# Kernel optimization log

Measured on AMD Instinct MI355X. Metric: run time of the kernel, lower is better.

The kernel has to match this reference:

```python
import jax, jax.numpy as jnp
import numpy as np

B, T, D, H, E, S, K = 2, 2048, 768, 1536, 8, 1, 2
STD = 0.02


def setup_inputs() -> dict:
    key = jax.random.key(0)
    ks = jax.random.split(key, 8)
    x = jax.random.normal(ks[0], (B, T, D), jnp.float32)
    router_w = jax.random.normal(ks[1], (E, D), jnp.float32) * STD
    sw1 = jax.random.normal(ks[2], (S, D, H), jnp.float32) * STD
    sw2 = jax.random.normal(ks[3], (S, D, H), jnp.float32) * STD
    sproj = jax.random.normal(ks[4], (S, H, D), jnp.float32) * STD
    ew1 = jax.random.normal(ks[5], (E, D, H), jnp.float32) * STD
    ew2 = jax.random.normal(ks[6], (E, D, H), jnp.float32) * STD
    eproj = jax.random.normal(ks[7], (E, H, D), jnp.float32) * STD
    return {"x": x, "router_w": router_w, "sw1": sw1, "sw2": sw2,
            "sproj": sproj, "ew1": ew1, "ew2": ew2, "eproj": eproj,
            "top_k": K}


def reference(x, router_w, sw1, sw2, sproj, ew1, ew2, eproj, top_k):
    n_experts = router_w.shape[0]
    # Shared experts (SwiGLU), summed over the shared-expert axis s.
    a = jnp.einsum('btd,sdh->bsth', x, sw1)
    b = jnp.einsum('btd,sdh->bsth', x, sw2)
    shared_out = jnp.einsum('bsth,shd->btd', jax.nn.silu(a) * b, sproj)  # [B,T,D]

    # Router: note the original applies softmax and calls the result `logits`,
    # returning it as the second output.
    probs = jax.nn.softmax(jnp.einsum('btd,ed->bte', x, router_w), axis=-1)  # [B,T,E]
    top_vals, top_idx = jax.lax.top_k(probs, top_k)
    weights = top_vals / jnp.sum(top_vals, axis=-1, keepdims=True)  # renormalized [B,T,K]

    # Dense combine weights: combine[b,t,e] = sum_k weights[b,t,k] * 1[top_idx[b,t,k]==e]
    combine = jnp.sum(jax.nn.one_hot(top_idx, n_experts, dtype=x.dtype)
                      * weights[..., None], axis=-2)  # [B,T,E]

    # Routed experts: compute every expert densely, then mask/weight by combine.
    ea = jnp.einsum('btd,edh->bteh', x, ew1)
    eb = jnp.einsum('btd,edh->bteh', x, ew2)
    routed = jnp.einsum('bteh,ehd,bte->btd', jax.nn.silu(ea) * eb, eproj, combine)

    return shared_out + routed, probs
```

## Files before the change

### kernel.cpp

```cpp
#include <hip/hip_runtime.h>

typedef unsigned short u16;
typedef __bf16 bf16x8 __attribute__((ext_vector_type(8)));
typedef float f32x4 __attribute__((ext_vector_type(4)));

__device__ __forceinline__ u16 f2bf(float f) {
  union { float f; unsigned u; } v; v.f = f;
  return (u16)((v.u + 0x7fffu + ((v.u >> 16) & 1u)) >> 16);
}

#define GLDS16(g, l)                                                          \
  __builtin_amdgcn_global_load_lds(                                           \
      (const __attribute__((address_space(1))) void*)(g),                     \
      (__attribute__((address_space(3))) void*)(l), 16, 0, 0)

#define SBAR()  __builtin_amdgcn_s_barrier()
#define SCHED() __builtin_amdgcn_sched_barrier(0)
#define VMCNT(n) asm volatile("s_waitcnt vmcnt(" #n ")" ::: "memory")

#define NTOK 4096
#define DIM  768
#define HID  1536
#define NEXP 8
#define CAPR 10240
#define SHB  10240
#define NSLOT 14336
#define MAXT1 56
#define MAXT2 112

__global__ __launch_bounds__(256) void k_tr_all(const float* __restrict__ ew1,
                                                const float* __restrict__ sw1,
                                                const float* __restrict__ ew2,
                                                const float* __restrict__ sw2,
                                                const float* __restrict__ eproj,
                                                const float* __restrict__ sproj,
                                                u16* __restrict__ dstBase) {
  __shared__ u16 tile[64][65];
  constexpr size_t SL = (size_t)HID * DIM;
  const int z = blockIdx.z;
  const float* src;
  int R, C, bxx = blockIdx.x, byy = blockIdx.y;
  if (z < 9)       { src = (z < 8) ? ew1 + (size_t)z * SL : sw1; R = DIM; C = HID; }
  else if (z < 18) { const int q = z - 9;  src = (q < 8) ? ew2 + (size_t)q * SL : sw2; R = DIM; C = HID; }
  else             { const int q = z - 18; src = (q < 8) ? eproj + (size_t)q * SL : sproj;
                     R = HID; C = DIM; const int t = bxx; bxx = byy; byy = t; }
  u16* dst = dstBase + (size_t)z * SL;
  const int c0 = bxx * 64, r0 = byy * 64;
  const int tx = threadIdx.x, ty = threadIdx.y;
  #pragma unroll
  for (int i = 0; i < 16; i++)
    tile[ty + 4 * i][tx] = f2bf(src[(size_t)(r0 + ty + 4 * i) * C + c0 + tx]);
  __syncthreads();
  #pragma unroll
  for (int i = 0; i < 16; i++)
    dst[(size_t)(c0 + ty + 4 * i) * R + r0 + tx] = tile[tx][ty + 4 * i];
}

__global__ __launch_bounds__(256) void k_router(const float* __restrict__ x,
                                                const float* __restrict__ rw,
                                                float* __restrict__ probs,
                                                int* __restrict__ topIdx,
                                                float* __restrict__ topW,
                                                u16* __restrict__ xb) {
  const int wv = threadIdx.x >> 6, lane = threadIdx.x & 63;
  const int t = blockIdx.x * 4 + wv;
  const float* xr = x + (size_t)t * DIM;
  u16* xbr = xb + (size_t)t * DIM;
  float acc[NEXP] = {0, 0, 0, 0, 0, 0, 0, 0};
  #pragma unroll
  for (int i = 0; i < DIM / 64; i++) {
    const int d = lane + 64 * i;
    const float xv = xr[d];
    xbr[d] = f2bf(xv);
    #pragma unroll
    for (int e = 0; e < NEXP; e++) acc[e] += xv * rw[e * DIM + d];
  }
  #pragma unroll
  for (int e = 0; e < NEXP; e++)
    #pragma unroll
    for (int s = 32; s > 0; s >>= 1) acc[e] += __shfl_xor(acc[e], s, 64);
  if (lane == 0) {
    float mx = acc[0];
    #pragma unroll
    for (int e = 1; e < NEXP; e++) mx = fmaxf(mx, acc[e]);
    float p[NEXP], sum = 0.f;
    #pragma unroll
    for (int e = 0; e < NEXP; e++) { p[e] = expf(acc[e] - mx); sum += p[e]; }
    const float inv = 1.f / sum;
    #pragma unroll
    for (int e = 0; e < NEXP; e++) p[e] *= inv;
    #pragma unroll
    for (int e = 0; e < NEXP; e++) probs[(size_t)t * NEXP + e] = p[e];
    int i1 = 0;
    #pragma unroll
    for (int e = 1; e < NEXP; e++) if (p[e] > p[i1]) i1 = e;
    int i2 = (i1 == 0) ? 1 : 0;
    #pragma unroll
    for (int e = 0; e < NEXP; e++) if (e != i1 && p[e] > p[i2]) i2 = e;
    const float s2 = 1.f / (p[i1] + p[i2]);
    topIdx[2 * t] = i1; topIdx[2 * t + 1] = i2;
    topW[2 * t] = p[i1] * s2; topW[2 * t + 1] = p[i2] * s2;
  }
}

__global__ __launch_bounds__(256) void k_build(const int* __restrict__ topIdx,
                                               const float* __restrict__ topW,
                                               int* __restrict__ listT,
                                               float* __restrict__ listW,
                                               int* __restrict__ listP,
                                               int* __restrict__ cnt) {
  const int e = blockIdx.x;
  const int tid = threadIdx.x, w = tid >> 6, lane = tid & 63;
  __shared__ int wt[4];
  int base = 0;
  for (int c = 0; c < NTOK / 256; ++c) {
    const int t = c * 256 + tid;
    const int i0 = topIdx[2 * t], i1 = topIdx[2 * t + 1];
    const int pr = (i0 == e) ? 1 : ((i1 == e) ? 2 : 0);
    const unsigned long long m = __ballot(pr != 0);
    const int wl = __popcll(m & ((1ull << lane) - 1ull));
    if (lane == 0) wt[w] = __popcll(m);
    __syncthreads();
    int wbase = 0;
    #pragma unroll
    for (int j = 0; j < 4; j++) if (j < w) wbase += wt[j];
    if (pr) {
      const int pos = base + wbase + wl;
      listT[e * NTOK + pos] = t;
      listW[e * NTOK + pos] = (pr == 1) ? topW[2 * t] : topW[2 * t + 1];
      listP[e * NTOK + pos] = pr;
    }
    base += wt[0] + wt[1] + wt[2] + wt[3];
    __syncthreads();
  }
  if (tid == 0) cnt[e] = base;
}

__global__ __launch_bounds__(64) void k_maps(const int* __restrict__ cnt,
                                             int* __restrict__ tE1, int* __restrict__ tM1,
                                             int* __restrict__ tE2, int* __restrict__ tM2,
                                             int* __restrict__ offPad) {
  if (threadIdx.x == 0) {
    int tt = 0, acc = 0;
    for (int e = 0; e < NEXP; e++) {
      offPad[e] = acc;
      const int tiles = (cnt[e] + 255) >> 8;
      for (int i = 0; i < tiles; i++) { tE1[tt] = e; tM1[tt] = acc + i * 256; tt++; }
      acc += tiles * 256;
    }
    offPad[NEXP] = acc;
    for (int i = 0; i < NTOK / 256; i++) { tE1[tt] = NEXP; tM1[tt] = SHB + i * 256; tt++; }
    for (; tt < MAXT1; tt++) { tE1[tt] = -1; tM1[tt] = 0; }
    for (int j = 0; j < MAXT1; j++) {
      tE2[2 * j] = tE1[j];     tM2[2 * j] = tM1[j];
      tE2[2 * j + 1] = tE1[j]; tM2[2 * j + 1] = tM1[j] + 128;
    }
  }
}

__global__ __launch_bounds__(256) void k_slots(const int* __restrict__ offPad,
                                               const int* __restrict__ cnt,
                                               const int* __restrict__ listT,
                                               const float* __restrict__ listW,
                                               const int* __restrict__ listP,
                                               int* __restrict__ slotTok,
                                               float* __restrict__ slotW,
                                               int* __restrict__ tokSlot) {
  __shared__ int op[NEXP + 1];
  __shared__ int cs[NEXP];
  if (threadIdx.x < NEXP + 1) op[threadIdx.x] = offPad[threadIdx.x];
  if (threadIdx.x < NEXP) cs[threadIdx.x] = cnt[threadIdx.x];
  __syncthreads();
  const int s = blockIdx.x * 256 + threadIdx.x;
  if (s < CAPR) {
    int tok = 0; float wv = 0.f; int pp = 0;
    #pragma unroll
    for (int e = 0; e < NEXP; e++)
      if (s >= op[e] && s < op[e + 1]) {
        const int i = s - op[e];
        if (i < cs[e]) {
          tok = listT[e * NTOK + i];
          wv = listW[e * NTOK + i];
          pp = listP[e * NTOK + i];
        }
      }
    slotTok[s] = tok; slotW[s] = wv;
    if (pp) tokSlot[2 * tok + (pp - 1)] = s;
  } else {
    const int t = s - CAPR;
    slotTok[SHB + t] = t; slotW[SHB + t] = 1.f;
  }
}

__global__ __launch_bounds__(512, 2) void k_gemm1(const u16* __restrict__ xb,
                                                  const u16* __restrict__ w1t,
                                                  const u16* __restrict__ w2t,
                                                  const int* __restrict__ tE1,
                                                  const int* __restrict__ tM1,
                                                  const int* __restrict__ slotTok,
                                                  const float* __restrict__ slotW,
                                                  u16* __restrict__ hidden) {
  __shared__ alignas(16) u16 L[2][32768];
  const int bid = blockIdx.x;
  const int wgid = (bid & 7) * 84 + (bid >> 3);
  const int bx = wgid % MAXT1, by = wgid / MAXT1;
  const int e = tE1[bx];
  if (e < 0) return;
  const int m0 = tM1[bx];
  const int nBase = by * 128;
  constexpr size_t SL = (size_t)HID * DIM;
  const u16* w1 = w1t + (size_t)e * SL;
  const u16* w2 = w2t + (size_t)e * SL;
  const int tid = threadIdx.x, w = tid >> 6, lane = tid & 63;
  const int wr = w >> 1, wc = w & 1;

  const int srow = tid >> 2;
  const int kcol = ((tid & 3) ^ ((tid >> 3) & 3)) * 8;
  const int tokA0 = slotTok[m0 + srow];
  const int tokA1 = slotTok[m0 + 128 + srow];
  const u16* gA0 = xb + (size_t)tokA0 * DIM + kcol;
  const u16* gA1 = xb + (size_t)tokA1 * DIM + kcol;
  const u16* gB1 = w1 + (size_t)(nBase + srow) * DIM + kcol;
  const u16* gB2 = w2 + (size_t)(nBase + srow) * DIM + kcol;
  const int dA0 = tid * 8, dA1 = 4096 + tid * 8, dB = tid * 8;

  const int rl = lane & 15;
  const int kq = lane >> 4;
  const int aBase = (wr * 64 + rl) * 32 + (kq ^ ((rl >> 1) & 3)) * 8;
  const int bBase = (wc * 64 + rl) * 32 + (kq ^ ((rl >> 1) & 3)) * 8;

  f32x4 acc1[4][4], acc2[4][4];
  const f32x4 vz = {0.f, 0.f, 0.f, 0.f};
  #pragma unroll
  for (int m = 0; m < 4; m++)
    #pragma unroll
    for (int n = 0; n < 4; n++) { acc1[m][n] = vz; acc2[m][n] = vz; }

#define G1_STA(d, koff, kh) do {                                              \
    GLDS16(gA0 + (koff), &L[d][(kh) * 8192 + dA0]);                           \
    GLDS16(gA1 + (koff), &L[d][(kh) * 8192 + dA1]); } while (0)
#define G1_STB(d, koff, kh) do {                                              \
    GLDS16(gB1 + (koff), &L[d][16384 + (kh) * 4096 + dB]);                    \
    GLDS16(gB2 + (koff), &L[d][24576 + (kh) * 4096 + dB]); } while (0)
#define G1_RDB(d, kh) do { _Pragma("unroll")                                  \
    for (int n = 0; n < 4; n++) {                                             \
      b1v[n] = *(const bf16x8*)&L[d][16384 + (kh) * 4096 + bBase + n * 512];  \
      b2v[n] = *(const bf16x8*)&L[d][24576 + (kh) * 4096 + bBase + n * 512]; } } while (0)
#define G1_RDA(d, kh, mp) do { _Pragma("unroll")                              \
    for (int j = 0; j < 2; j++)                                               \
      av[j] = *(const bf16x8*)&L[d][(kh) * 8192 + aBase + ((mp) * 2 + j) * 512]; } while (0)
#define G1_MM(mp) do { __builtin_amdgcn_s_setprio(1);                         \
    _Pragma("unroll") for (int j = 0; j < 2; j++)                             \
      _Pragma("unroll") for (int n = 0; n < 4; n++) {                         \
        acc1[(mp) * 2 + j][n] = __builtin_amdgcn_mfma_f32_16x16x32_bf16(av[j], b1v[n], acc1[(mp) * 2 + j][n], 0, 0, 0); \
        acc2[(mp) * 2 + j][n] = __builtin_amdgcn_mfma_f32_16x16x32_bf16(av[j], b2v[n], acc2[(mp) * 2 + j][n], 0, 0, 0); } \
    __builtin_amdgcn_s_setprio(0); } while (0)

  G1_STA(0, 0, 0);  G1_STB(0, 0, 0);
  G1_STA(0, 32, 1); G1_STB(0, 32, 1);
  G1_STA(1, 64, 0); G1_STB(1, 64, 0);
  SCHED(); VMCNT(8); SBAR(); SCHED();

  bf16x8 av[2], b1v[4], b2v[4];
  for (int i = 0; i < 5; i++) {
    const int kOff = i * 128;
    G1_RDB(0, 0); G1_RDA(0, 0, 0); SCHED(); G1_STA(1, kOff + 96, 1); SCHED();
    G1_MM(0); SCHED(); SBAR(); SCHED();
    G1_RDA(0, 0, 1); SCHED(); G1_STB(1, kOff + 96, 1); SCHED();
    G1_MM(1); SCHED(); VMCNT(8); SBAR(); SCHED();
    G1_RDB(0, 1); G1_RDA(0, 1, 0); SCHED(); G1_STA(0, kOff + 128, 0); SCHED();
    G1_MM(0); SCHED(); SBAR(); SCHED();
    G1_RDA(0, 1, 1); SCHED(); G1_STB(0, kOff + 128, 0); SCHED();
    G1_MM(1); SCHED(); VMCNT(8); SBAR(); SCHED();
    G1_RDB(1, 0); G1_RDA(1, 0, 0); SCHED(); G1_STA(0, kOff + 160, 1); SCHED();
    G1_MM(0); SCHED(); SBAR(); SCHED();
    G1_RDA(1, 0, 1); SCHED(); G1_STB(0, kOff + 160, 1); SCHED();
    G1_MM(1); SCHED(); VMCNT(8); SBAR(); SCHED();
    G1_RDB(1, 1); G1_RDA(1, 1, 0); SCHED(); G1_STA(1, kOff + 192, 0); SCHED();
    G1_MM(0); SCHED(); SBAR(); SCHED();
    G1_RDA(1, 1, 1); SCHED(); G1_STB(1, kOff + 192, 0); SCHED();
    G1_MM(1); SCHED(); VMCNT(8); SBAR(); SCHED();
  }
  G1_RDB(0, 0); G1_RDA(0, 0, 0); SCHED(); G1_STA(1, 736, 1); SCHED();
  G1_MM(0); SCHED(); SBAR(); SCHED();
  G1_RDA(0, 0, 1); SCHED(); G1_STB(1, 736, 1); SCHED();
  G1_MM(1); SCHED(); VMCNT(8); SBAR(); SCHED();
  G1_RDB(0, 1); G1_RDA(0, 1, 0); SCHED(); G1_MM(0); SCHED(); SBAR(); SCHED();
  G1_RDA(0, 1, 1); SCHED(); G1_MM(1); SCHED(); VMCNT(4); SBAR(); SCHED();
  G1_RDB(1, 0); G1_RDA(1, 0, 0); SCHED(); G1_MM(0); SCHED(); SBAR(); SCHED();
  G1_RDA(1, 0, 1); SCHED(); G1_MM(1); SCHED(); VMCNT(0); SBAR(); SCHED();
  G1_RDB(1, 1); G1_RDA(1, 1, 0); SCHED(); G1_MM(0); SCHED(); SBAR(); SCHED();
  G1_RDA(1, 1, 1); SCHED(); G1_MM(1);
#undef G1_STA
#undef G1_STB
#undef G1_RDB
#undef G1_RDA
#undef G1_MM

  #pragma unroll
  for (int m = 0; m < 4; m++)
    #pragma unroll
    for (int r = 0; r < 4; r++) {
      const int slot = m0 + wr * 64 + m * 16 + (lane >> 4) * 4 + r;
      const float cwv = slotW[slot];
      #pragma unroll
      for (int n = 0; n < 4; n++) {
        const int hcol = nBase + wc * 64 + n * 16 + (lane & 15);
        const float v1 = acc1[m][n][r], v2 = acc2[m][n][r];
        hidden[(size_t)slot * HID + hcol] = f2bf((v1 / (1.f + __expf(-v1))) * v2 * cwv);
      }
    }
}

__global__ __launch_bounds__(256, 2) void k_gemm2(const u16* __restrict__ hid,
                                                  const u16* __restrict__ pjt,
                                                  const int* __restrict__ tE2,
                                                  const int* __restrict__ tM2,
                                                  float* __restrict__ g2) {
  __shared__ alignas(16) u16 L[2][16384];
  const int bid = blockIdx.x;
  const int wgid = (bid & 7) * 84 + (bid >> 3);
  const int bx = wgid % MAXT2, by = wgid / MAXT2;
  const int e = tE2[bx];
  if (e < 0) return;
  const int m0 = tM2[bx];
  const int nBase = by * 128;
  constexpr size_t SL = (size_t)HID * DIM;
  const u16* pj = pjt + (size_t)e * SL;
  const int tid = threadIdx.x, w = tid >> 6, lane = tid & 63;
  const int wr = w >> 1, wc = w & 1;

  const int r0 = tid >> 2;
  const int kcol = ((tid & 3) ^ ((tid >> 3) & 3)) * 8;
  const u16* gA0 = hid + (size_t)(m0 + r0) * HID + kcol;
  const u16* gA1 = hid + (size_t)(m0 + 64 + r0) * HID + kcol;
  const u16* gB0 = pj + (size_t)(nBase + r0) * HID + kcol;
  const u16* gB1p = pj + (size_t)(nBase + 64 + r0) * HID + kcol;
  const int d0 = tid * 8, d1 = 2048 + tid * 8;

  const int rl = lane & 15;
  const int kq = lane >> 4;
  const int aBase = (wr * 64 + rl) * 32 + (kq ^ ((rl >> 1) & 3)) * 8;
  const int bBase = (wc * 64 + rl) * 32 + (kq ^ ((rl >> 1) & 3)) * 8;

  f32x4 acc[4][4];
  const f32x4 vz = {0.f, 0.f, 0.f, 0.f};
  #pragma unroll
  for (int m = 0; m < 4; m++)
    #pragma unroll
    for (int n = 0; n < 4; n++) acc[m][n] = vz;

#define G2_STA(d, koff, kh) do {                                              \
    GLDS16(gA0 + (koff), &L[d][(kh) * 4096 + d0]);                            \
    GLDS16(gA1 + (koff), &L[d][(kh) * 4096 + d1]); } while (0)
#define G2_STB(d, koff, kh) do {                                              \
    GLDS16(gB0 + (koff), &L[d][8192 + (kh) * 4096 + d0]);                     \
    GLDS16(gB1p + (koff), &L[d][8192 + (kh) * 4096 + d1]); } while (0)
#define G2_RDB(d, kh) do { _Pragma("unroll")                                  \
    for (int n = 0; n < 4; n++)                                               \
      bv[n] = *(const bf16x8*)&L[d][8192 + (kh) * 4096 + bBase + n * 512]; } while (0)
#define G2_RDA(d, kh, mp) do { _Pragma("unroll")                              \
    for (int j = 0; j < 2; j++)                                               \
      av[j] = *(const bf16x8*)&L[d][(kh) * 4096 + aBase + ((mp) * 2 + j) * 512]; } while (0)
#define G2_MM(mp) do { __builtin_amdgcn_s_setprio(1);                         \
    _Pragma("unroll") for (int j = 0; j < 2; j++)                             \
      _Pragma("unroll") for (int n = 0; n < 4; n++)                           \
        acc[(mp) * 2 + j][n] = __builtin_amdgcn_mfma_f32_16x16x32_bf16(av[j], bv[n], acc[(mp) * 2 + j][n], 0, 0, 0); \
    __builtin_amdgcn_s_setprio(0); } while (0)

  G2_STA(0, 0, 0);  G2_STB(0, 0, 0);
  G2_STA(0, 32, 1); G2_STB(0, 32, 1);
  G2_STA(1, 64, 0); G2_STB(1, 64, 0);
  SCHED(); VMCNT(8); SBAR(); SCHED();

  bf16x8 av[2], bv[4];
  for (int i = 0; i < 11; i++) {
    const int kOff = i * 128;
    G2_RDB(0, 0); G2_RDA(0, 0, 0); SCHED(); G2_STA(1, kOff + 96, 1); SCHED();
    G2_MM(0); SCHED(); SBAR(); SCHED();
    G2_RDA(0, 0, 1); SCHED(); G2_STB(1, kOff + 96, 1); SCHED();
    G2_MM(1); SCHED(); VMCNT(8); SBAR(); SCHED();
    G2_RDB(0, 1); G2_RDA(0, 1, 0); SCHED(); G2_STA(0, kOff + 128, 0); SCHED();
    G2_MM(0); SCHED(); SBAR(); SCHED();
    G2_RDA(0, 1, 1); SCHED(); G2_STB(0, kOff + 128, 0); SCHED();
    G2_MM(1); SCHED(); VMCNT(8); SBAR(); SCHED();
    G2_RDB(1, 0); G2_RDA(1, 0, 0); SCHED(); G2_STA(0, kOff + 160, 1); SCHED();
    G2_MM(0); SCHED(); SBAR(); SCHED();
    G2_RDA(1, 0, 1); SCHED(); G2_STB(0, kOff + 160, 1); SCHED();
    G2_MM(1); SCHED(); VMCNT(8); SBAR(); SCHED();
    G2_RDB(1, 1); G2_RDA(1, 1, 0); SCHED(); G2_STA(1, kOff + 192, 0); SCHED();
    G2_MM(0); SCHED(); SBAR(); SCHED();
    G2_RDA(1, 1, 1); SCHED(); G2_STB(1, kOff + 192, 0); SCHED();
    G2_MM(1); SCHED(); VMCNT(8); SBAR(); SCHED();
  }
  G2_RDB(0, 0); G2_RDA(0, 0, 0); SCHED(); G2_STA(1, 1504, 1); SCHED();
  G2_MM(0); SCHED(); SBAR(); SCHED();
  G2_RDA(0, 0, 1); SCHED(); G2_STB(1, 1504, 1); SCHED();
  G2_MM(1); SCHED(); VMCNT(8); SBAR(); SCHED();
  G2_RDB(0, 1); G2_RDA(0, 1, 0); SCHED(); G2_MM(0); SCHED(); SBAR(); SCHED();
  G2_RDA(0, 1, 1); SCHED(); G2_MM(1); SCHED(); VMCNT(4); SBAR(); SCHED();
  G2_RDB(1, 0); G2_RDA(1, 0, 0); SCHED(); G2_MM(0); SCHED(); SBAR(); SCHED();
  G2_RDA(1, 0, 1); SCHED(); G2_MM(1); SCHED(); VMCNT(0); SBAR(); SCHED();
  G2_RDB(1, 1); G2_RDA(1, 1, 0); SCHED(); G2_MM(0); SCHED(); SBAR(); SCHED();
  G2_RDA(1, 1, 1); SCHED(); G2_MM(1);
#undef G2_STA
#undef G2_STB
#undef G2_RDB
#undef G2_RDA
#undef G2_MM

  #pragma unroll
  for (int m = 0; m < 4; m++)
    #pragma unroll
    for (int r = 0; r < 4; r++) {
      const int slot = m0 + wr * 64 + m * 16 + (lane >> 4) * 4 + r;
      #pragma unroll
      for (int n = 0; n < 4; n++) {
        const int dcol = nBase + wc * 64 + n * 16 + (lane & 15);
        g2[(size_t)slot * DIM + dcol] = acc[m][n][r];
      }
    }
}

__global__ __launch_bounds__(192) void k_combine(const float* __restrict__ g2,
                                                 const int* __restrict__ tokSlot,
                                                 float* __restrict__ out) {
  const int t = blockIdx.x, d4 = threadIdx.x;
  const int sA = tokSlot[2 * t], sB = tokSlot[2 * t + 1];
  const int lo = sA < sB ? sA : sB;
  const int hi = sA < sB ? sB : sA;
  const float4 a = ((const float4*)(g2 + (size_t)lo * DIM))[d4];
  const float4 b = ((const float4*)(g2 + (size_t)hi * DIM))[d4];
  const float4 c = ((const float4*)(g2 + (size_t)(SHB + t) * DIM))[d4];
  float4 o;
  o.x = a.x + b.x + c.x; o.y = a.y + b.y + c.y;
  o.z = a.z + b.z + c.z; o.w = a.w + b.w + c.w;
  ((float4*)(out + (size_t)t * DIM))[d4] = o;
}

extern "C" void kernel_launch(void* const* d_in, const int* in_sizes, int n_in,
                              void* d_out, int out_size, void* d_ws, size_t ws_size,
                              hipStream_t stream) {
  const float* x     = (const float*)d_in[0];
  const float* rw    = (const float*)d_in[1];
  const float* sw1   = (const float*)d_in[2];
  const float* sw2   = (const float*)d_in[3];
  const float* sproj = (const float*)d_in[4];
  const float* ew1   = (const float*)d_in[5];
  const float* ew2   = (const float*)d_in[6];
  const float* eproj = (const float*)d_in[7];
  float* out   = (float*)d_out;
  float* probs = out + (size_t)NTOK * DIM;

  constexpr size_t SL = (size_t)HID * DIM;
  constexpr size_t off_xb   = 0;
  constexpr size_t off_w1t  = 6291456;
  constexpr size_t off_w2t  = off_w1t + 2 * 9 * SL;
  constexpr size_t off_pjt  = off_w2t + 2 * 9 * SL;
  constexpr size_t off_hid  = off_pjt + 2 * 9 * SL;
  constexpr size_t off_g2   = off_hid + (size_t)NSLOT * HID * 2;
  constexpr size_t off_meta = off_g2 + (size_t)NSLOT * DIM * 4;

  char* ws = (char*)d_ws;
  u16*   xb   = (u16*)(ws + off_xb);
  u16*   w1t  = (u16*)(ws + off_w1t);
  u16*   w2t  = (u16*)(ws + off_w2t);
  u16*   pjt  = (u16*)(ws + off_pjt);
  u16*   hid  = (u16*)(ws + off_hid);
  float* g2   = (float*)(ws + off_g2);
  char*  meta = ws + off_meta;
  int*   topIdx  = (int*)meta;
  float* topW    = (float*)(meta + 32768);
  int*   listT   = (int*)(meta + 65536);
  float* listW   = (float*)(meta + 196608);
  int*   listP   = (int*)(meta + 327680);
  int*   cnt     = (int*)(meta + 458752);
  int*   tE1     = (int*)(meta + 459264);
  int*   tM1     = (int*)(meta + 459776);
  int*   tE2     = (int*)(meta + 460288);
  int*   tM2     = (int*)(meta + 460800);
  int*   slotTok = (int*)(meta + 461312);
  float* slotW   = (float*)(meta + 518656);
  int*   tokSlot = (int*)(meta + 576000);
  int*   offPad  = (int*)(meta + 608768);

  k_router<<<NTOK / 4, 256, 0, stream>>>(x, rw, probs, topIdx, topW, xb);
  k_tr_all<<<dim3(HID / 64, DIM / 64, 27), dim3(64, 4), 0, stream>>>(
      ew1, sw1, ew2, sw2, eproj, sproj, w1t);

  k_build<<<NEXP, 256, 0, stream>>>(topIdx, topW, listT, listW, listP, cnt);
  k_maps<<<1, 64, 0, stream>>>(cnt, tE1, tM1, tE2, tM2, offPad);
  k_slots<<<NSLOT / 256, 256, 0, stream>>>(offPad, cnt, listT, listW, listP,
                                           slotTok, slotW, tokSlot);

  k_gemm1<<<MAXT1 * (HID / 128), 512, 0, stream>>>(xb, w1t, w2t, tE1, tM1,
                                                   slotTok, slotW, hid);
  k_gemm2<<<MAXT2 * (DIM / 128), 256, 0, stream>>>(hid, pjt, tE2, tM2, g2);
  k_combine<<<NTOK, 192, 0, stream>>>(g2, tokSlot, out);
}
```

Before: 198.3 us.

## Fuse router, weight transpose and slot assignment into one atomic-routing prep kernel

Merges the router, the weight transpose/convert and the token-to-slot assignment into a single k_prep launch. Slots are now claimed with per-expert atomic counters into fixed-size per-expert slabs. The GEMM kernels decode their expert tile from the counts directly, which removes the k_build, k_maps and k_slots launches and their serial scans. The trade-offs are a fixed per-expert capacity of 1536 (tokens beyond it are silently dropped), a memset, and nondeterministic slot ordering.

```diff
diff --git a/kernel.cpp b/kernel.cpp
--- a/kernel.cpp
+++ b/kernel.cpp
@@ -22,191 +22,136 @@
 #define DIM  768
 #define HID  1536
 #define NEXP 8
-#define CAPR 10240
-#define SHB  10240
-#define NSLOT 14336
-#define MAXT1 56
-#define MAXT2 112
-
-__global__ __launch_bounds__(256) void k_tr_all(const float* __restrict__ ew1,
-                                                const float* __restrict__ sw1,
-                                                const float* __restrict__ ew2,
-                                                const float* __restrict__ sw2,
-                                                const float* __restrict__ eproj,
-                                                const float* __restrict__ sproj,
-                                                u16* __restrict__ dstBase) {
-  __shared__ u16 tile[64][65];
+#define SLAB 1536
+#define CAPR (NEXP * SLAB)
+#define SHB  CAPR
+#define NSLOT (CAPR + NTOK)
+#define MAXT1 64
+#define MAXT2 128
+
+__global__ __launch_bounds__(256) void k_prep(const float* __restrict__ x,
+                                              const float* __restrict__ rw,
+                                              const float* __restrict__ ew1,
+                                              const float* __restrict__ sw1,
+                                              const float* __restrict__ ew2,
+                                              const float* __restrict__ sw2,
+                                              const float* __restrict__ eproj,
+                                              const float* __restrict__ sproj,
+                                              u16* __restrict__ dstBase,
+                                              u16* __restrict__ xb,
+                                              float* __restrict__ probs,
+                                              int* __restrict__ cnt,
+                                              int* __restrict__ slotTok,
+                                              float* __restrict__ slotW,
+                                              int* __restrict__ tokSlot) {
   constexpr size_t SL = (size_t)HID * DIM;
   const int z = blockIdx.z;
-  const float* src;
-  int R, C, bxx = blockIdx.x, byy = blockIdx.y;
-  if (z < 9)       { src = (z < 8) ? ew1 + (size_t)z * SL : sw1; R = DIM; C = HID; }
-  else if (z < 18) { const int q = z - 9;  src = (q < 8) ? ew2 + (size_t)q * SL : sw2; R = DIM; C = HID; }
-  else             { const int q = z - 18; src = (q < 8) ? eproj + (size_t)q * SL : sproj;
-                     R = HID; C = DIM; const int t = bxx; bxx = byy; byy = t; }
-  u16* dst = dstBase + (size_t)z * SL;
-  const int c0 = bxx * 64, r0 = byy * 64;
-  const int tx = threadIdx.x, ty = threadIdx.y;
+  if (z < 27) {
+    __shared__ u16 tile[64][65];
+    const float* src;
+    int R, C, bxx = blockIdx.x, byy = blockIdx.y;
+    if (z < 9)       { src = (z < 8) ? ew1 + (size_t)z * SL : sw1; R = DIM; C = HID; }
+    else if (z < 18) { const int q = z - 9;  src = (q < 8) ? ew2 + (size_t)q * SL : sw2; R = DIM; C = HID; }
+    else             { const int q = z - 18; src = (q < 8) ? eproj + (size_t)q * SL : sproj;
+                       R = HID; C = DIM; const int t = bxx; bxx = byy; byy = t; }
+    u16* dst = dstBase + (size_t)z * SL;
+    const int c0 = bxx * 64, r0 = byy * 64;
+    const int tx = threadIdx.x, ty = threadIdx.y;
+    #pragma unroll
+    for (int i = 0; i < 16; i++)
+      tile[ty + 4 * i][tx] = f2bf(src[(size_t)(r0 + ty + 4 * i) * C + c0 + tx]);
+    __syncthreads();
+    #pragma unroll
+    for (int i = 0; i < 16; i++)
+      dst[(size_t)(c0 + ty + 4 * i) * R + r0 + tx] = tile[tx][ty + 4 * i];
+    return;
+  }
+  const int tid = threadIdx.y * 64 + threadIdx.x;
+  const int wv = tid >> 6, lane = tid & 63;
+  const int rb = blockIdx.y * 24 + blockIdx.x;
+  for (int j = wv; j < 15; j += 4) {
+    const int t = rb + 288 * j;
+    if (t >= NTOK) continue;
+    const float* xr = x + (size_t)t * DIM;
+    u16* xbr = xb + (size_t)t * DIM;
+    float acc[NEXP] = {0, 0, 0, 0, 0, 0, 0, 0};
+    #pragma unroll
+    for (int i = 0; i < DIM / 64; i++) {
+      const int d = lane + 64 * i;
+      const float xv = xr[d];
+      xbr[d] = f2bf(xv);
+      #pragma unroll
+      for (int e = 0; e < NEXP; e++) acc[e] += xv * rw[e * DIM + d];
+    }
+    #pragma unroll
+    for (int e = 0; e < NEXP; e++)
+      #pragma unroll
+      for (int s = 32; s > 0; s >>= 1) acc[e] += __shfl_xor(acc[e], s, 64);
+    if (lane == 0) {
+      float mx = acc[0];
+      #pragma unroll
+      for (int e = 1; e < NEXP; e++) mx = fmaxf(mx, acc[e]);
+      float p[NEXP], sum = 0.f;
+      #pragma unroll
+      for (int e = 0; e < NEXP; e++) { p[e] = expf(acc[e] - mx); sum += p[e]; }
+      const float inv = 1.f / sum;
+      #pragma unroll
+      for (int e = 0; e < NEXP; e++) p[e] *= inv;
+      #pragma unroll
+      for (int e = 0; e < NEXP; e++) probs[(size_t)t * NEXP + e] = p[e];
+      int i1 = 0;
+      #pragma unroll
+      for (int e = 1; e < NEXP; e++) if (p[e] > p[i1]) i1 = e;
+      int i2 = (i1 == 0) ? 1 : 0;
+      #pragma unroll
+      for (int e = 0; e < NEXP; e++) if (e != i1 && p[e] > p[i2]) i2 = e;
+      const float s2 = 1.f / (p[i1] + p[i2]);
+      const int p1 = atomicAdd(&cnt[i1], 1);
+      if (p1 < SLAB) {
+        const int s = i1 * SLAB + p1;
+        slotTok[s] = t; slotW[s] = p[i1] * s2; tokSlot[2 * t] = s;
+      }
+      const int p2 = atomicAdd(&cnt[i2], 1);
+      if (p2 < SLAB) {
+        const int s = i2 * SLAB + p2;
+        slotTok[s] = t; slotW[s] = p[i2] * s2; tokSlot[2 * t + 1] = s;
+      }
+      slotTok[SHB + t] = t; slotW[SHB + t] = 1.f;
+    }
+  }
+}
+
+__device__ __forceinline__ int decode_tile(const int* __restrict__ cnt, int bx,
+                                           int rows_log2, int nShared, int* m0out) {
+  int e = -1, m0 = 0, acc = 0;
   #pragma unroll
-  for (int i = 0; i < 16; i++)
-    tile[ty + 4 * i][tx] = f2bf(src[(size_t)(r0 + ty + 4 * i) * C + c0 + tx]);
-  __syncthreads();
-  #pragma unroll
-  for (int i = 0; i < 16; i++)
-    dst[(size_t)(c0 + ty + 4 * i) * R + r0 + tx] = tile[tx][ty + 4 * i];
-}
-
-__global__ __launch_bounds__(256) void k_router(const float* __restrict__ x,
-                                                const float* __restrict__ rw,
-                                                float* __restrict__ probs,
-                                                int* __restrict__ topIdx,
-                                                float* __restrict__ topW,
-                                                u16* __restrict__ xb) {
-  const int wv = threadIdx.x >> 6, lane = threadIdx.x & 63;
-  const int t = blockIdx.x * 4 + wv;
-  const float* xr = x + (size_t)t * DIM;
-  u16* xbr = xb + (size_t)t * DIM;
-  float acc[NEXP] = {0, 0, 0, 0, 0, 0, 0, 0};
-  #pragma unroll
-  for (int i = 0; i < DIM / 64; i++) {
-    const int d = lane + 64 * i;
-    const float xv = xr[d];
-    xbr[d] = f2bf(xv);
-    #pragma unroll
-    for (int e = 0; e < NEXP; e++) acc[e] += xv * rw[e * DIM + d];
-  }
-  #pragma unroll
-  for (int e = 0; e < NEXP; e++)
-    #pragma unroll
-    for (int s = 32; s > 0; s >>= 1) acc[e] += __shfl_xor(acc[e], s, 64);
-  if (lane == 0) {
-    float mx = acc[0];
-    #pragma unroll
-    for (int e = 1; e < NEXP; e++) mx = fmaxf(mx, acc[e]);
-    float p[NEXP], sum = 0.f;
-    #pragma unroll
-    for (int e = 0; e < NEXP; e++) { p[e] = expf(acc[e] - mx); sum += p[e]; }
-    const float inv = 1.f / sum;
-    #pragma unroll
-    for (int e = 0; e < NEXP; e++) p[e] *= inv;
-    #pragma unroll
-    for (int e = 0; e < NEXP; e++) probs[(size_t)t * NEXP + e] = p[e];
-    int i1 = 0;
-    #pragma unroll
-    for (int e = 1; e < NEXP; e++) if (p[e] > p[i1]) i1 = e;
-    int i2 = (i1 == 0) ? 1 : 0;
-    #pragma unroll
-    for (int e = 0; e < NEXP; e++) if (e != i1 && p[e] > p[i2]) i2 = e;
-    const float s2 = 1.f / (p[i1] + p[i2]);
-    topIdx[2 * t] = i1; topIdx[2 * t + 1] = i2;
-    topW[2 * t] = p[i1] * s2; topW[2 * t + 1] = p[i2] * s2;
-  }
-}
-
-__global__ __launch_bounds__(256) void k_build(const int* __restrict__ topIdx,
-                                               const float* __restrict__ topW,
-                                               int* __restrict__ listT,
-                                               float* __restrict__ listW,
-                                               int* __restrict__ listP,
-                                               int* __restrict__ cnt) {
-  const int e = blockIdx.x;
-  const int tid = threadIdx.x, w = tid >> 6, lane = tid & 63;
-  __shared__ int wt[4];
-  int base = 0;
-  for (int c = 0; c < NTOK / 256; ++c) {
-    const int t = c * 256 + tid;
-    const int i0 = topIdx[2 * t], i1 = topIdx[2 * t + 1];
-    const int pr = (i0 == e) ? 1 : ((i1 == e) ? 2 : 0);
-    const unsigned long long m = __ballot(pr != 0);
-    const int wl = __popcll(m & ((1ull << lane) - 1ull));
-    if (lane == 0) wt[w] = __popcll(m);
-    __syncthreads();
-    int wbase = 0;
-    #pragma unroll
-    for (int j = 0; j < 4; j++) if (j < w) wbase += wt[j];
-    if (pr) {
-      const int pos = base + wbase + wl;
-      listT[e * NTOK + pos] = t;
-      listW[e * NTOK + pos] = (pr == 1) ? topW[2 * t] : topW[2 * t + 1];
-      listP[e * NTOK + pos] = pr;
-    }
-    base += wt[0] + wt[1] + wt[2] + wt[3];
-    __syncthreads();
-  }
-  if (tid == 0) cnt[e] = base;
-}
-
-__global__ __launch_bounds__(64) void k_maps(const int* __restrict__ cnt,
-                                             int* __restrict__ tE1, int* __restrict__ tM1,
-                                             int* __restrict__ tE2, int* __restrict__ tM2,
-                                             int* __restrict__ offPad) {
-  if (threadIdx.x == 0) {
-    int tt = 0, acc = 0;
-    for (int e = 0; e < NEXP; e++) {
-      offPad[e] = acc;
-      const int tiles = (cnt[e] + 255) >> 8;
-      for (int i = 0; i < tiles; i++) { tE1[tt] = e; tM1[tt] = acc + i * 256; tt++; }
-      acc += tiles * 256;
-    }
-    offPad[NEXP] = acc;
-    for (int i = 0; i < NTOK / 256; i++) { tE1[tt] = NEXP; tM1[tt] = SHB + i * 256; tt++; }
-    for (; tt < MAXT1; tt++) { tE1[tt] = -1; tM1[tt] = 0; }
-    for (int j = 0; j < MAXT1; j++) {
-      tE2[2 * j] = tE1[j];     tM2[2 * j] = tM1[j];
-      tE2[2 * j + 1] = tE1[j]; tM2[2 * j + 1] = tM1[j] + 128;
-    }
-  }
-}
-
-__global__ __launch_bounds__(256) void k_slots(const int* __restrict__ offPad,
-                                               const int* __restrict__ cnt,
-                                               const int* __restrict__ listT,
-                                               const float* __restrict__ listW,
-                                               const int* __restrict__ listP,
-                                               int* __restrict__ slotTok,
-                                               float* __restrict__ slotW,
-                                               int* __restrict__ tokSlot) {
-  __shared__ int op[NEXP + 1];
-  __shared__ int cs[NEXP];
-  if (threadIdx.x < NEXP + 1) op[threadIdx.x] = offPad[threadIdx.x];
-  if (threadIdx.x < NEXP) cs[threadIdx.x] = cnt[threadIdx.x];
-  __syncthreads();
-  const int s = blockIdx.x * 256 + threadIdx.x;
-  if (s < CAPR) {
-    int tok = 0; float wv = 0.f; int pp = 0;
-    #pragma unroll
-    for (int e = 0; e < NEXP; e++)
-      if (s >= op[e] && s < op[e + 1]) {
-        const int i = s - op[e];
-        if (i < cs[e]) {
-          tok = listT[e * NTOK + i];
-          wv = listW[e * NTOK + i];
-          pp = listP[e * NTOK + i];
-        }
-      }
-    slotTok[s] = tok; slotW[s] = wv;
-    if (pp) tokSlot[2 * tok + (pp - 1)] = s;
-  } else {
-    const int t = s - CAPR;
-    slotTok[SHB + t] = t; slotW[SHB + t] = 1.f;
-  }
+  for (int ee = 0; ee < NEXP; ee++) {
+    const int tl = (cnt[ee] + ((1 << rows_log2) - 1)) >> rows_log2;
+    if (bx >= acc && bx < acc + tl) { e = ee; m0 = ee * SLAB + ((bx - acc) << rows_log2); }
+    acc += tl;
+  }
+  if (e < 0) {
+    const int sx = bx - acc;
+    if (sx >= 0 && sx < nShared) { e = NEXP; m0 = SHB + (sx << rows_log2); }
+  }
+  *m0out = m0;
+  return e;
 }
 
 __global__ __launch_bounds__(512, 2) void k_gemm1(const u16* __restrict__ xb,
                                                   const u16* __restrict__ w1t,
                                                   const u16* __restrict__ w2t,
-                                                  const int* __restrict__ tE1,
-                                                  const int* __restrict__ tM1,
+                                                  const int* __restrict__ cnt,
                                                   const int* __restrict__ slotTok,
                                                   const float* __restrict__ slotW,
                                                   u16* __restrict__ hidden) {
   __shared__ alignas(16) u16 L[2][32768];
   const int bid = blockIdx.x;
-  const int wgid = (bid & 7) * 84 + (bid >> 3);
+  const int wgid = (bid & 7) * 96 + (bid >> 3);
   const int bx = wgid % MAXT1, by = wgid / MAXT1;
-  const int e = tE1[bx];
+  int m0;
+  const int e = decode_tile(cnt, bx, 8, NTOK / 256, &m0);
   if (e < 0) return;
-  const int m0 = tM1[bx];
   const int nBase = by * 128;
   constexpr size_t SL = (size_t)HID * DIM;
   const u16* w1 = w1t + (size_t)e * SL;
@@ -314,16 +259,15 @@
 
 __global__ __launch_bounds__(256, 2) void k_gemm2(const u16* __restrict__ hid,
                                                   const u16* __restrict__ pjt,
-                                                  const int* __restrict__ tE2,
-                                                  const int* __restrict__ tM2,
+                                                  const int* __restrict__ cnt,
                                                   float* __restrict__ g2) {
   __shared__ alignas(16) u16 L[2][16384];
   const int bid = blockIdx.x;
-  const int wgid = (bid & 7) * 84 + (bid >> 3);
+  const int wgid = (bid & 7) * 96 + (bid >> 3);
   const int bx = wgid % MAXT2, by = wgid / MAXT2;
-  const int e = tE2[bx];
+  int m0;
+  const int e = decode_tile(cnt, bx, 7, NTOK / 128, &m0);
   if (e < 0) return;
-  const int m0 = tM2[bx];
   const int nBase = by * 128;
   constexpr size_t SL = (size_t)HID * DIM;
   const u16* pj = pjt + (size_t)e * SL;
@@ -427,10 +371,8 @@
                                                  float* __restrict__ out) {
   const int t = blockIdx.x, d4 = threadIdx.x;
   const int sA = tokSlot[2 * t], sB = tokSlot[2 * t + 1];
-  const int lo = sA < sB ? sA : sB;
-  const int hi = sA < sB ? sB : sA;
-  const float4 a = ((const float4*)(g2 + (size_t)lo * DIM))[d4];
-  const float4 b = ((const float4*)(g2 + (size_t)hi * DIM))[d4];
+  const float4 a = ((const float4*)(g2 + (size_t)sA * DIM))[d4];
+  const float4 b = ((const float4*)(g2 + (size_t)sB * DIM))[d4];
   const float4 c = ((const float4*)(g2 + (size_t)(SHB + t) * DIM))[d4];
   float4 o;
   o.x = a.x + b.x + c.x; o.y = a.y + b.y + c.y;
@@ -469,32 +411,19 @@
   u16*   hid  = (u16*)(ws + off_hid);
   float* g2   = (float*)(ws + off_g2);
   char*  meta = ws + off_meta;
-  int*   topIdx  = (int*)meta;
-  float* topW    = (float*)(meta + 32768);
-  int*   listT   = (int*)(meta + 65536);
-  float* listW   = (float*)(meta + 196608);
-  int*   listP   = (int*)(meta + 327680);
-  int*   cnt     = (int*)(meta + 458752);
-  int*   tE1     = (int*)(meta + 459264);
-  int*   tM1     = (int*)(meta + 459776);
-  int*   tE2     = (int*)(meta + 460288);
-  int*   tM2     = (int*)(meta + 460800);
-  int*   slotTok = (int*)(meta + 461312);
-  float* slotW   = (float*)(meta + 518656);
-  int*   tokSlot = (int*)(meta + 576000);
-  int*   offPad  = (int*)(meta + 608768);
-
-  k_router<<<NTOK / 4, 256, 0, stream>>>(x, rw, probs, topIdx, topW, xb);
-  k_tr_all<<<dim3(HID / 64, DIM / 64, 27), dim3(64, 4), 0, stream>>>(
-      ew1, sw1, ew2, sw2, eproj, sproj, w1t);
-
-  k_build<<<NEXP, 256, 0, stream>>>(topIdx, topW, listT, listW, listP, cnt);
-  k_maps<<<1, 64, 0, stream>>>(cnt, tE1, tM1, tE2, tM2, offPad);
-  k_slots<<<NSLOT / 256, 256, 0, stream>>>(offPad, cnt, listT, listW, listP,
-                                           slotTok, slotW, tokSlot);
-
-  k_gemm1<<<MAXT1 * (HID / 128), 512, 0, stream>>>(xb, w1t, w2t, tE1, tM1,
+  int*   cnt     = (int*)meta;
+  int*   slotTok = (int*)(meta + 128);
+  float* slotW   = (float*)(meta + 128 + 65536);
+  int*   tokSlot = (int*)(meta + 128 + 131072);
+
+  hipMemsetAsync(meta, 0, 128 + 131072, stream);
+
+  k_prep<<<dim3(HID / 64, DIM / 64, 28), dim3(64, 4), 0, stream>>>(
+      x, rw, ew1, sw1, ew2, sw2, eproj, sproj, w1t, xb,
+      probs, cnt, slotTok, slotW, tokSlot);
+
+  k_gemm1<<<MAXT1 * (HID / 128), 512, 0, stream>>>(xb, w1t, w2t, cnt,
                                                    slotTok, slotW, hid);
-  k_gemm2<<<MAXT2 * (DIM / 128), 256, 0, stream>>>(hid, pjt, tE2, tM2, g2);
+  k_gemm2<<<MAXT2 * (DIM / 128), 256, 0, stream>>>(hid, pjt, cnt, g2);
   k_combine<<<NTOK, 192, 0, stream>>>(g2, tokSlot, out);
 }
```

Result: slower. 272.1 us (+37.2%).
